# Kernel optimization log

Measured on AMD Instinct MI355X. Metric: run time of the kernel, lower is better.

## Reference

```python
import jax, jax.numpy as jnp
import numpy as np

PAD_POS = 100.0   # column 0: sigmoid(100) ~ 1  (identity factor on left)
PAD_NEG = -100.0  # column 1: 1 - sigmoid(-100) ~ 1 (identity factor on right)


def setup_inputs() -> dict:
    key = jax.random.key(0)
    k1, k2 = jax.random.split(key)
    B, V = 2048, 32768
    scores = jax.random.normal(k1, (B, V), dtype=jnp.float32)
    class_indices = jax.random.randint(k2, (B,), 0, V, dtype=jnp.int64)
    return {"scores": scores, "class_indices": class_indices}


def _tree_indices(class_indices, code_len):
    """Vectorized version of the host-side per-bit tree traversal.
    Returns left_t, right_t of shape [B, code_len] (int32 gather indices)."""
    ci = class_indices.astype(jnp.int32)
    shifts = jnp.arange(code_len - 1, -1, -1, dtype=jnp.int32)
    bits = (ci[:, None] >> shifts[None, :]) & 1  # [B, L], MSB first

    def step(idx, bit):  # idx: [B] current tree node index into padded_scores
        right_branch = bit == 1
        left = jnp.where(right_branch, 0, idx)    # 0 -> sigmoid(100) ~ 1
        right = jnp.where(right_branch, idx, 1)   # 1 -> 1 - sigmoid(-100) ~ 1
        nidx = jnp.where(right_branch, 2 * idx, 2 * idx - 1)
        return nidx, (left, right)

    init = jnp.full(ci.shape, 2, dtype=jnp.int32)
    _, (left_t, right_t) = jax.lax.scan(step, init, bits.T)  # [L, B]
    return left_t.T, right_t.T


def reference(scores, class_indices):
    B, V = scores.shape
    code_len = int(np.ceil(np.log2(V)))
    padded = jnp.concatenate(
        [jnp.full((B, 1), PAD_POS, scores.dtype),
         jnp.full((B, 1), PAD_NEG, scores.dtype),
         scores], axis=1)  # [B, V+2]
    left_t, right_t = _tree_indices(class_indices, code_len)  # [B, L]
    left_part = jax.nn.sigmoid(jnp.take_along_axis(padded, left_t, axis=1))
    right_part = 1.0 - jax.nn.sigmoid(jnp.take_along_axis(padded, right_t, axis=1))
    probs = jnp.prod(left_part, axis=1) * jnp.prod(right_part, axis=1)  # [B]
    return jnp.sum(-jnp.log(probs)) / B
```

## Files before the change

### kernel.cpp

```cpp
#include <hip/hip_runtime.h>


#define B_ROWS   2048
#define V_COLS   32768
#define CODE_LEN 15

__device__ __forceinline__ float softplus_f(float x) {
    return fmaxf(x, 0.0f) + log1pf(expf(-fabsf(x)));
}

__global__ void hsm_partial_kernel(const float* __restrict__ scores,
                                   const int* __restrict__ class_indices,
                                   float* __restrict__ partials) {
    const int b = blockIdx.x * blockDim.x + threadIdx.x;
    float acc = 0.0f;
    if (b < B_ROWS) {
        const int ci = class_indices[b];
        const float* row = scores + (size_t)b * V_COLS;
        int idx = 2;
#pragma unroll
        for (int shift = CODE_LEN - 1; shift >= 0; --shift) {
            const int bit = (ci >> shift) & 1;
            const float s = row[idx - 2];
            acc += softplus_f(bit ? s : -s);
            idx = bit ? (2 * idx) : (2 * idx - 1);
        }
    }
#pragma unroll
    for (int off = 32; off > 0; off >>= 1)
        acc += __shfl_down(acc, off);
    if (threadIdx.x == 0)
        partials[blockIdx.x] = acc;
}

__global__ void hsm_final_kernel(const float* __restrict__ partials,
                                 float* __restrict__ out,
                                 int n_partials) {
    float acc = (threadIdx.x < n_partials) ? partials[threadIdx.x] : 0.0f;
#pragma unroll
    for (int off = 32; off > 0; off >>= 1)
        acc += __shfl_down(acc, off);
    if (threadIdx.x == 0)
        out[0] = acc * (1.0f / (float)B_ROWS);
}

extern "C" void kernel_launch(void* const* d_in, const int* in_sizes, int n_in,
                              void* d_out, int out_size, void* d_ws, size_t ws_size,
                              hipStream_t stream) {
    const float* scores        = (const float*)d_in[0];
    const int*   class_indices = (const int*)d_in[1];
    float*       out           = (float*)d_out;
    float*       partials      = (float*)d_ws;

    const int threads = 64;
    const int blocks  = B_ROWS / threads;

    hsm_partial_kernel<<<blocks, threads, 0, stream>>>(scores, class_indices, partials);
    hsm_final_kernel<<<1, 64, 0, stream>>>(partials, out, blocks);
}
```

Before: 11.20 us.

## Fuse partial and final reduction via atomicAdd; compute tree indices in closed form

Drops the second reduction kernel: each block atomically adds its scaled partial sum into the output, which is zeroed with an async memset beforehand. The tree node index for each level is now computed in closed form from the class index, which removes the serial index dependency and lets all 15 loads issue independently. The cost is a memset launch plus float atomic ordering, which makes the result nondeterministic in its last bits.

```diff
diff --git a/kernel.cpp b/kernel.cpp
--- a/kernel.cpp
+++ b/kernel.cpp
@@ -9,39 +9,27 @@
     return fmaxf(x, 0.0f) + log1pf(expf(-fabsf(x)));
 }
 
-__global__ void hsm_partial_kernel(const float* __restrict__ scores,
-                                   const int* __restrict__ class_indices,
-                                   float* __restrict__ partials) {
+__global__ void hsm_fused_kernel(const float* __restrict__ scores,
+                                 const int* __restrict__ class_indices,
+                                 float* __restrict__ out) {
     const int b = blockIdx.x * blockDim.x + threadIdx.x;
+    const int ci = class_indices[b];
+    const float* row = scores + (size_t)b * V_COLS;
+
     float acc = 0.0f;
-    if (b < B_ROWS) {
-        const int ci = class_indices[b];
-        const float* row = scores + (size_t)b * V_COLS;
-        int idx = 2;
 #pragma unroll
-        for (int shift = CODE_LEN - 1; shift >= 0; --shift) {
-            const int bit = (ci >> shift) & 1;
-            const float s = row[idx - 2];
-            acc += softplus_f(bit ? s : -s);
-            idx = bit ? (2 * idx) : (2 * idx - 1);
-        }
+    for (int t = 0; t < CODE_LEN; ++t) {
+        const float s = row[((1 << t) - 1) + (ci >> (CODE_LEN - t))];
+        const int bit = (ci >> (CODE_LEN - 1 - t)) & 1;
+        acc += softplus_f(bit ? s : -s);
     }
+
 #pragma unroll
     for (int off = 32; off > 0; off >>= 1)
         acc += __shfl_down(acc, off);
+
     if (threadIdx.x == 0)
-        partials[blockIdx.x] = acc;
-}
-
-__global__ void hsm_final_kernel(const float* __restrict__ partials,
-                                 float* __restrict__ out,
-                                 int n_partials) {
-    float acc = (threadIdx.x < n_partials) ? partials[threadIdx.x] : 0.0f;
-#pragma unroll
-    for (int off = 32; off > 0; off >>= 1)
-        acc += __shfl_down(acc, off);
-    if (threadIdx.x == 0)
-        out[0] = acc * (1.0f / (float)B_ROWS);
+        atomicAdd(out, acc * (1.0f / (float)B_ROWS));
 }
 
 extern "C" void kernel_launch(void* const* d_in, const int* in_sizes, int n_in,
@@ -50,11 +38,10 @@
     const float* scores        = (const float*)d_in[0];
     const int*   class_indices = (const int*)d_in[1];
     float*       out           = (float*)d_out;
-    float*       partials      = (float*)d_ws;
+
+    hipMemsetAsync(out, 0, sizeof(float), stream);
 
     const int threads = 64;
     const int blocks  = B_ROWS / threads;
-
-    hsm_partial_kernel<<<blocks, threads, 0, stream>>>(scores, class_indices, partials);
-    hsm_final_kernel<<<1, 64, 0, stream>>>(partials, out, blocks);
+    hsm_fused_kernel<<<blocks, threads, 0, stream>>>(scores, class_indices, out);
 }
```

Measured after the change: 14.81 us. +32.3%, slower.
